# Kernel optimization log

Measured on AMD Instinct MI355X. Metric: run time of the kernel, lower is better.

Reference implementation:

```python
import jax, jax.numpy as jnp
import numpy as np

H, DK, DV, S = 16, 1024, 1024, 2048
DH_QK = DK // H  # 64, per-head q/k dim
DH_V = DV // H   # 64, per-head v dim


def setup_inputs() -> dict:
    key = jax.random.key(0)
    ks = jax.random.split(key, 11)
    init = lambda k, shape, fan_in: jax.random.uniform(k, shape, jnp.float32, -1.0, 1.0) / jnp.sqrt(jnp.float32(fan_in))
    return {
        "Q": jax.random.normal(ks[0], (S, DK), jnp.float32),
        "K": jax.random.normal(ks[1], (S, DK), jnp.float32),
        "V": jax.random.normal(ks[2], (S, DV), jnp.float32),
        # per-head Linear weights, torch convention [out, in] stacked over heads
        "Wq": init(ks[3], (H, DH_QK, DH_QK), DH_QK),
        "bq": init(ks[4], (H, DH_QK), DH_QK),
        "Wk": init(ks[5], (H, DH_QK, DH_QK), DH_QK),
        "bk": init(ks[6], (H, DH_QK), DH_QK),
        "Wv": init(ks[7], (H, DH_V, DH_V), DH_V),
        "bv": init(ks[8], (H, DH_V), DH_V),
        "Wo": init(ks[9], (DK, H * DH_V), H * DH_V),  # final linear: d_model x (h*dv_h)
        "bo": init(ks[10], (DK,), H * DH_V),
    }


def reference(Q, K, V, Wq, bq, Wk, bk, Wv, bv, Wo, bo):
    h, dh = Wq.shape[0], Wq.shape[2]
    dv = Wv.shape[2]
    s = Q.shape[0]
    # split features into h per-head chunks (same as slicing loop in torch)
    Qh = Q.reshape(s, h, dh)
    Kh = K.reshape(s, h, dh)
    Vh = V.reshape(s, h, dv)
    # per-head Linear: x @ W.T + b, batched over heads
    q = jnp.einsum('shd,hed->she', Qh, Wq) + bq
    k = jnp.einsum('shd,hed->she', Kh, Wk) + bk
    v = jnp.einsum('shd,hed->she', Vh, Wv) + bv
    # scaled dot-product attention per head
    scores = jnp.einsum('she,the->hst', q, k) / jnp.sqrt(jnp.float32(dh))
    attn = jax.nn.softmax(scores, axis=-1)
    o = jnp.einsum('hst,the->she', attn, v)  # [s, h, dv]
    concat = o.reshape(s, h * dv)
    return concat @ Wo.T + bo
```

## Files before the change

kernel.cpp:

```cpp
#include <hip/hip_runtime.h>
#include <stdint.h>

static constexpr int H   = 16;
static constexpr int S   = 2048;
static constexpr int DHd = 64;
static constexpr int DM  = 1024;
static constexpr int NSPLIT = 4;
static constexpr int KT_PER_SPLIT = (S / 64) / NSPLIT;

using f32x4   = __attribute__((ext_vector_type(4))) float;
using f32x8   = __attribute__((ext_vector_type(8))) float;
using f32x16  = __attribute__((ext_vector_type(16))) float;
using short8  = __attribute__((ext_vector_type(8))) short;
using bf16x8  = __attribute__((ext_vector_type(8))) __bf16;
using uint4v  = __attribute__((ext_vector_type(4))) unsigned int;

#if __has_builtin(__builtin_amdgcn_exp2f)
#define EXP2F __builtin_amdgcn_exp2f
#else
#define EXP2F exp2f
#endif

__device__ __forceinline__ short f2bf(float f) {
  union { float f; uint32_t u; } v; v.f = f;
  uint32_t r = v.u + 0x7FFFu + ((v.u >> 16) & 1u);
  return (short)(r >> 16);
}
__device__ __forceinline__ float bf2f(short s) {
  union { uint32_t u; float f; } v;
  v.u = ((uint32_t)(unsigned short)s) << 16;
  return v.f;
}

__device__ __forceinline__ short8 f2bf8(f32x4 a, f32x4 b) {
  short8 v;
  v[0] = f2bf(a[0]); v[1] = f2bf(a[1]); v[2] = f2bf(a[2]); v[3] = f2bf(a[3]);
  v[4] = f2bf(b[0]); v[5] = f2bf(b[1]); v[6] = f2bf(b[2]); v[7] = f2bf(b[3]);
  return v;
}

__device__ __forceinline__ unsigned int pkbf(float a, float b) {
  __bf16 x = (__bf16)a, y = (__bf16)b;
  unsigned short ux = __builtin_bit_cast(unsigned short, x);
  unsigned short uy = __builtin_bit_cast(unsigned short, y);
  return (unsigned int)ux | ((unsigned int)uy << 16);
}

__device__ __forceinline__ f32x4 mfma16(short8 a, short8 b, f32x4 c) {
  return __builtin_amdgcn_mfma_f32_16x16x32_bf16(
      __builtin_bit_cast(bf16x8, a), __builtin_bit_cast(bf16x8, b), c, 0, 0, 0);
}
__device__ __forceinline__ f32x16 mfma32(short8 a, short8 b, f32x16 c) {
  return __builtin_amdgcn_mfma_f32_32x32x16_bf16(
      __builtin_bit_cast(bf16x8, a), __builtin_bit_cast(bf16x8, b), c, 0, 0, 0);
}

__device__ __forceinline__ short8 lds_read_swz(const short* base, int row, int chunk) {
  return *(const short8*)((const char*)base + row * 128 + ((chunk ^ (row & 7)) << 4));
}
__device__ __forceinline__ void lds_write_swz(short* base, int row, int chunk, short8 v) {
  *(short8*)((char*)base + row * 128 + ((chunk ^ (row & 7)) << 4)) = v;
}

using u32g = __attribute__((address_space(1))) const unsigned int;
using u32l = __attribute__((address_space(3))) unsigned int;
__device__ __forceinline__ void gl_lds16(const short* g, short* l) {
  __builtin_amdgcn_global_load_lds(
      reinterpret_cast<u32g*>(reinterpret_cast<uintptr_t>(g)),
      reinterpret_cast<u32l*>(static_cast<unsigned int>(reinterpret_cast<uintptr_t>(l))),
      16, 0, 0);
}

__global__ __launch_bounds__(256) void proj_kernel(
    const float* __restrict__ Q, const float* __restrict__ K, const float* __restrict__ V,
    const float* __restrict__ Wq, const float* __restrict__ bq,
    const float* __restrict__ Wk, const float* __restrict__ bk,
    const float* __restrict__ Wv, const float* __restrict__ bv,
    const float* __restrict__ Wo, short* __restrict__ wob,
    short* __restrict__ qb, short* __restrict__ kb, short* __restrict__ vtb) {
  const int t = threadIdx.x;
  const int mode = blockIdx.z;

  if (mode == 3) {
    int chunk = blockIdx.y * gridDim.x + blockIdx.x;
    int i = (chunk * 256 + t) * 16;
    f32x4 x0 = *(const f32x4*)(Wo + i);
    f32x4 x1 = *(const f32x4*)(Wo + i + 4);
    f32x4 x2 = *(const f32x4*)(Wo + i + 8);
    f32x4 x3 = *(const f32x4*)(Wo + i + 12);
    *(short8*)(wob + i)     = f2bf8(x0, x1);
    *(short8*)(wob + i + 8) = f2bf8(x2, x3);
    return;
  }

  const int h  = blockIdx.y;
  const int rt = blockIdx.x * 128;

  const float* X; const float* W; const float* bias;
  if (mode == 0)      { X = Q; W = Wq; bias = bq; }
  else if (mode == 1) { X = K; W = Wk; bias = bk; }
  else                { X = V; W = Wv; bias = bv; }
  bias += h * DHd;
  const float scale = (mode == 0) ? 0.125f * 1.44269504f : 1.0f;

  __shared__ short Xs[128 * 64];
  __shared__ short Ws[64 * 64];
  __shared__ short Ot[128 * 72];

#pragma unroll
  for (int p = 0; p < 4; p++) {
    int ci = p * 256 + t;
    int row = ci >> 3, oct = ci & 7;
    const float* g = X + (size_t)(rt + row) * DM + h * DHd + oct * 8;
    f32x4 x0 = *(const f32x4*)g;
    f32x4 x1 = *(const f32x4*)(g + 4);
    lds_write_swz(Xs, row, oct, f2bf8(x0, x1));
  }
#pragma unroll
  for (int p = 0; p < 2; p++) {
    int ci = p * 256 + t;
    int row = ci >> 3, oct = ci & 7;
    const float* g = W + (size_t)h * DHd * DHd + row * DHd + oct * 8;
    f32x4 x0 = *(const f32x4*)g;
    f32x4 x1 = *(const f32x4*)(g + 4);
    lds_write_swz(Ws, row, oct, f2bf8(x0, x1));
  }
  __syncthreads();

  const int wid = t >> 6, lane = t & 63;
  const int l15 = lane & 15, l4 = lane >> 4;

  f32x4 acc[2][4] = {};
#pragma unroll
  for (int ks = 0; ks < 2; ks++) {
    int chunk = ks * 4 + l4;
    short8 a0 = lds_read_swz(Xs, wid * 32 + l15, chunk);
    short8 a1 = lds_read_swz(Xs, wid * 32 + 16 + l15, chunk);
#pragma unroll
    for (int nf = 0; nf < 4; nf++) {
      short8 b = lds_read_swz(Ws, nf * 16 + l15, chunk);
      acc[0][nf] = mfma16(a0, b, acc[0][nf]);
      acc[1][nf] = mfma16(a1, b, acc[1][nf]);
    }
  }

  if (mode < 2) {
    short* out = (mode == 0) ? qb : kb;
#pragma unroll
    for (int mf = 0; mf < 2; mf++)
#pragma unroll
      for (int nf = 0; nf < 4; nf++) {
        int col = nf * 16 + l15;
        float b = bias[col];
#pragma unroll
        for (int r = 0; r < 4; r++) {
          int lrow = wid * 32 + mf * 16 + l4 * 4 + r;
          Ot[lrow * 72 + col] = f2bf((acc[mf][nf][r] + b) * scale);
        }
      }
    __syncthreads();
#pragma unroll
    for (int p = 0; p < 4; p++) {
      int ci = p * 256 + t;
      int row = ci >> 3, c8 = ci & 7;
      short8 v = *(const short8*)&Ot[row * 72 + c8 * 8];
      *(short8*)(out + ((size_t)h * S + rt + row) * DHd + c8 * 8) = v;
    }
  } else {
#pragma unroll
    for (int mf = 0; mf < 2; mf++)
#pragma unroll
      for (int nf = 0; nf < 4; nf++) {
        int col = nf * 16 + l15;
        float b = bias[col];
#pragma unroll
        for (int r = 0; r < 4; r++) {
          int lrow = wid * 32 + mf * 16 + l4 * 4 + r;
          Ot[col * 136 + lrow] = f2bf(acc[mf][nf][r] + b);
        }
      }
    __syncthreads();
#pragma unroll
    for (int p = 0; p < 2; p++) {
      int ci = p * 256 + t;
      int e = ci >> 3, c16 = ci & 7;
      short8 a = *(const short8*)&Ot[e * 136 + c16 * 16];
      short8 b = *(const short8*)&Ot[e * 136 + c16 * 16 + 8];
      short8 lo, hi;
      lo[0] = a[0]; lo[1] = a[1]; lo[2] = a[2]; lo[3] = a[3];
      lo[4] = b[0]; lo[5] = b[1]; lo[6] = b[2]; lo[7] = b[3];
      hi[0] = a[4]; hi[1] = a[5]; hi[2] = a[6]; hi[3] = a[7];
      hi[4] = b[4]; hi[5] = b[5]; hi[6] = b[6]; hi[7] = b[7];
      short* dst = vtb + ((size_t)h * DHd + e) * S + rt + c16 * 16;
      *(short8*)dst       = lo;
      *(short8*)(dst + 8) = hi;
    }
  }
}

__global__ __launch_bounds__(256, 2) void attn_kernel(
    const short* __restrict__ qb, const short* __restrict__ kb,
    const short* __restrict__ vtb, short* __restrict__ OpT,
    float* __restrict__ lbuf) {
  const int h  = blockIdx.x;
  const int sp = blockIdx.y;
  const int t = threadIdx.x, wid = t >> 6, lane = t & 63;
  const int l31 = lane & 31, l5 = lane >> 5;
  const int qw = blockIdx.z * 256 + wid * 64;

  __shared__ short Ks[3][64 * 64];
  __shared__ short Vs[3][64 * 64];

  short8 qf[2][4];
#pragma unroll
  for (int tt = 0; tt < 2; tt++) {
    const short* qrow = qb + ((size_t)h * S + qw + tt * 32 + l31) * DHd;
#pragma unroll
    for (int c = 0; c < 4; c++) qf[tt][c] = *(const short8*)(qrow + c * 16 + l5 * 8);
  }

  const int srow8 = lane >> 3, schunk = lane & 7;
  const int r0 = wid * 16 + srow8, r1 = r0 + 8;
  const int kt0 = sp * KT_PER_SPLIT;
  const short* kg0 = kb + ((size_t)h * S + (size_t)kt0 * 64 + r0) * DHd + ((schunk ^ (r0 & 7)) * 8);
  const short* kg1 = kb + ((size_t)h * S + (size_t)kt0 * 64 + r1) * DHd + ((schunk ^ (r1 & 7)) * 8);
  const short* vg0 = vtb + ((size_t)h * DHd + r0) * S + (size_t)kt0 * 64 + ((schunk ^ (r0 & 7)) * 8);
  const short* vg1 = vtb + ((size_t)h * DHd + r1) * S + (size_t)kt0 * 64 + ((schunk ^ (r1 & 7)) * 8);

  auto stage = [&](int buf, int kk) {
    const size_t ka = (size_t)kk * 64 * DHd;
    const size_t va = (size_t)kk * 64;
    gl_lds16(kg0 + ka, &Ks[buf][wid * 1024]);
    gl_lds16(kg1 + ka, &Ks[buf][wid * 1024 + 512]);
    gl_lds16(vg0 + va, &Vs[buf][wid * 1024]);
    gl_lds16(vg1 + va, &Vs[buf][wid * 1024 + 512]);
  };

  stage(0, 0);
  stage(1, 1);

  f32x16 oa00 = {}, oa01 = {}, oa10 = {}, oa11 = {};
  f32x8 lac0 = {}, lac1 = {};

  for (int kk = 0; kk < KT_PER_SPLIT; kk++) {
    const int cur = kk % 3;
    if (kk + 1 < KT_PER_SPLIT) asm volatile("s_waitcnt vmcnt(4)" ::: "memory");
    else                       asm volatile("s_waitcnt vmcnt(0)" ::: "memory");
    __syncthreads();
    if (kk + 2 < KT_PER_SPLIT) stage((kk + 2) % 3, kk + 2);

    f32x16 s00 = {}, s01 = {}, s10 = {}, s11 = {};
    __builtin_amdgcn_s_setprio(1);
#pragma unroll
    for (int c = 0; c < 4; c++) {
      short8 ak0 = lds_read_swz(Ks[cur], l31, 2 * c + l5);
      short8 ak1 = lds_read_swz(Ks[cur], 32 + l31, 2 * c + l5);
      s00 = mfma32(ak0, qf[0][c], s00);
      s01 = mfma32(ak1, qf[0][c], s01);
      s10 = mfma32(ak0, qf[1][c], s10);
      s11 = mfma32(ak1, qf[1][c], s11);
    }
    __builtin_amdgcn_s_setprio(0);

#pragma unroll
    for (int i = 0; i < 16; i++) {
      float p00 = EXP2F(s00[i]), p01 = EXP2F(s01[i]);
      float p10 = EXP2F(s10[i]), p11 = EXP2F(s11[i]);
      s00[i] = p00; s01[i] = p01; s10[i] = p10; s11[i] = p11;
      lac0[i & 7] += p00 + p01;
      lac1[i & 7] += p10 + p11;
    }

    unsigned int pk0[2][8], pk1[2][8];
#pragma unroll
    for (int g = 0; g < 4; g++) {
      pk0[0][g * 2 + 0] = pkbf(s00[4 * g + 0], s00[4 * g + 1]);
      pk0[0][g * 2 + 1] = pkbf(s00[4 * g + 2], s00[4 * g + 3]);
      pk0[1][g * 2 + 0] = pkbf(s01[4 * g + 0], s01[4 * g + 1]);
      pk0[1][g * 2 + 1] = pkbf(s01[4 * g + 2], s01[4 * g + 3]);
      pk1[0][g * 2 + 0] = pkbf(s10[4 * g + 0], s10[4 * g + 1]);
      pk1[0][g * 2 + 1] = pkbf(s10[4 * g + 2], s10[4 * g + 3]);
      pk1[1][g * 2 + 0] = pkbf(s11[4 * g + 0], s11[4 * g + 1]);
      pk1[1][g * 2 + 1] = pkbf(s11[4 * g + 2], s11[4 * g + 3]);
    }

    __builtin_amdgcn_s_setprio(1);
#pragma unroll
    for (int j = 0; j < 4; j++) {
      const int bb = j >> 1;
      const int s4 = (j & 1) * 4;
      short8 av0 = lds_read_swz(Vs[cur], l31, 2 * j + l5);
      short8 av1 = lds_read_swz(Vs[cur], 32 + l31, 2 * j + l5);
      uint4v pf0, pf1;
      pf0[0] = pk0[bb][s4 + 0]; pf0[1] = pk0[bb][s4 + 1];
      pf0[2] = pk0[bb][s4 + 2]; pf0[3] = pk0[bb][s4 + 3];
      pf1[0] = pk1[bb][s4 + 0]; pf1[1] = pk1[bb][s4 + 1];
      pf1[2] = pk1[bb][s4 + 2]; pf1[3] = pk1[bb][s4 + 3];
      short8 p0 = __builtin_bit_cast(short8, pf0);
      short8 p1 = __builtin_bit_cast(short8, pf1);
      oa00 = mfma32(av0, p0, oa00);
      oa01 = mfma32(av1, p0, oa01);
      oa10 = mfma32(av0, p1, oa10);
      oa11 = mfma32(av1, p1, oa11);
    }
    __builtin_amdgcn_s_setprio(0);
  }

#pragma unroll
  for (int st = 4; st >= 1; st >>= 1)
#pragma unroll
    for (int i = 0; i < st; i++) { lac0[i] += lac0[i + st]; lac1[i] += lac1[i + st]; }
  float l0 = lac0[0] + __shfl_xor(lac0[0], 32);
  float l1 = lac1[0] + __shfl_xor(lac1[0], 32);

#pragma unroll
  for (int r = 0; r < 16; r++) {
    int dvb = (r & 3) + 8 * (r >> 2) + 4 * l5;
    size_t base = (((size_t)sp * H + h) * DHd + dvb) * S + qw + l31;
    OpT[base]            = f2bf(oa00[r]);
    OpT[base + 32UL * S] = f2bf(oa01[r]);
    OpT[base + 32]            = f2bf(oa10[r]);
    OpT[base + 32UL * S + 32] = f2bf(oa11[r]);
  }
  if (l5 == 0) {
    lbuf[((size_t)sp * H + h) * S + qw + l31]      = l0;
    lbuf[((size_t)sp * H + h) * S + qw + 32 + l31] = l1;
  }
}

__global__ __launch_bounds__(256) void combine_kernel(
    const short* __restrict__ OpT, const float* __restrict__ lbuf,
    short* __restrict__ Ob) {
  const int h  = blockIdx.y;
  const int s0 = blockIdx.x * 64;
  __shared__ short tile[64][72];

  const int t = threadIdx.x;
  const int dvh = t >> 3;
  const int sb  = (t & 7) * 8;

  float lt[8] = {};
#pragma unroll
  for (int sp = 0; sp < NSPLIT; sp++) {
    const float* lp = lbuf + ((size_t)sp * H + h) * S + s0 + sb;
    f32x4 a = *(const f32x4*)lp;
    f32x4 b = *(const f32x4*)(lp + 4);
#pragma unroll
    for (int i = 0; i < 4; i++) { lt[i] += a[i]; lt[4 + i] += b[i]; }
  }
  float inv[8];
#pragma unroll
  for (int i = 0; i < 8; i++) inv[i] = 1.0f / lt[i];

#pragma unroll
  for (int half = 0; half < 2; half++) {
    const int dv = dvh + half * 32;
    float acc[8] = {};
#pragma unroll
    for (int sp = 0; sp < NSPLIT; sp++) {
      const short* op = OpT + (((size_t)sp * H + h) * DHd + dv) * S + s0 + sb;
      short8 v = *(const short8*)op;
#pragma unroll
      for (int i = 0; i < 8; i++) acc[i] += bf2f(v[i]);
    }
#pragma unroll
    for (int i = 0; i < 8; i++)
      tile[sb + i][dv] = f2bf(acc[i] * inv[i]);
  }
  __syncthreads();

#pragma unroll
  for (int i = 0; i < 2; i++) {
    int cid = t + i * 256;
    int r = cid >> 3, c = cid & 7;
    short8 v = *(const short8*)&tile[r][c * 8];
    *(short8*)(Ob + (size_t)(s0 + r) * DM + h * DHd + c * 8) = v;
  }
}

__global__ __launch_bounds__(256) void out_gemm(
    const short* __restrict__ Ob, const short* __restrict__ wob,
    const float* __restrict__ bo, float* __restrict__ out) {
  const int m0 = blockIdx.x * 64;
  const int n0 = blockIdx.y * 64;
  constexpr int KT = DM / 64;

  __shared__ short As[3][64 * 64];
  __shared__ short Bs[3][64 * 64];

  const int t = threadIdx.x, wid = t >> 6, lane = t & 63;
  const int l31 = lane & 31, l5 = lane >> 5;
  const int wr = wid >> 1, wn = wid & 1;
  const int srow8 = lane >> 3, schunk = lane & 7;
  const int r0 = wid * 16 + srow8, r1 = r0 + 8;

  const short* ag0 = Ob  + (size_t)(m0 + r0) * DM + ((schunk ^ (r0 & 7)) * 8);
  const short* ag1 = Ob  + (size_t)(m0 + r1) * DM + ((schunk ^ (r1 & 7)) * 8);
  const short* bg0 = wob + (size_t)(n0 + r0) * DM + ((schunk ^ (r0 & 7)) * 8);
  const short* bg1 = wob + (size_t)(n0 + r1) * DM + ((schunk ^ (r1 & 7)) * 8);

  auto stage = [&](int buf, int kc) {
    const int off = kc * 64;
    gl_lds16(ag0 + off, &As[buf][wid * 1024]);
    gl_lds16(ag1 + off, &As[buf][wid * 1024 + 512]);
    gl_lds16(bg0 + off, &Bs[buf][wid * 1024]);
    gl_lds16(bg1 + off, &Bs[buf][wid * 1024 + 512]);
  };

  stage(0, 0);
  stage(1, 1);

  f32x16 acc = {};
  for (int kc = 0; kc < KT; kc++) {
    const int cur = kc % 3;
    if (kc + 1 < KT) asm volatile("s_waitcnt vmcnt(4)" ::: "memory");
    else             asm volatile("s_waitcnt vmcnt(0)" ::: "memory");
    __syncthreads();
    if (kc + 2 < KT) stage((kc + 2) % 3, kc + 2);
#pragma unroll
    for (int c = 0; c < 4; c++) {
      short8 a = lds_read_swz(As[cur], wr * 32 + l31, 2 * c + l5);
      short8 b = lds_read_swz(Bs[cur], wn * 32 + l31, 2 * c + l5);
      acc = mfma32(a, b, acc);
    }
  }
  const int col = n0 + wn * 32 + l31;
  const float bb = bo[col];
#pragma unroll
  for (int r = 0; r < 16; r++) {
    int row = m0 + wr * 32 + (r & 3) + 8 * (r >> 2) + 4 * l5;
    out[(size_t)row * DM + col] = acc[r] + bb;
  }
}

extern "C" void kernel_launch(void* const* d_in, const int* in_sizes, int n_in,
                              void* d_out, int out_size, void* d_ws, size_t ws_size,
                              hipStream_t stream) {
  const float* Q  = (const float*)d_in[0];
  const float* K  = (const float*)d_in[1];
  const float* V  = (const float*)d_in[2];
  const float* Wq = (const float*)d_in[3];
  const float* bq = (const float*)d_in[4];
  const float* Wk = (const float*)d_in[5];
  const float* bk = (const float*)d_in[6];
  const float* Wv = (const float*)d_in[7];
  const float* bv = (const float*)d_in[8];
  const float* Wo = (const float*)d_in[9];
  const float* bo = (const float*)d_in[10];

  char* ws = (char*)d_ws;
  short* qb   = (short*)(ws);
  short* kb   = (short*)(ws + ((size_t)4 << 20));
  short* vtb  = (short*)(ws + ((size_t)8 << 20));
  short* Obf  = (short*)(ws + ((size_t)12 << 20));
  short* wob  = (short*)(ws + ((size_t)16 << 20));
  short* OpT  = (short*)(ws + ((size_t)18 << 20));
  float* lbuf = (float*)(ws + ((size_t)34 << 20));

  proj_kernel<<<dim3(S / 128, H, 4), 256, 0, stream>>>(Q, K, V, Wq, bq, Wk, bk, Wv, bv,
                                                       Wo, wob, qb, kb, vtb);
  attn_kernel<<<dim3(H, NSPLIT, S / 256), 256, 0, stream>>>(qb, kb, vtb, OpT, lbuf);
  combine_kernel<<<dim3(S / 64, H), 256, 0, stream>>>(OpT, lbuf, Obf);
  out_gemm<<<dim3(S / 64, DM / 64), 256, 0, stream>>>(Obf, wob, bo, (float*)d_out);
}
```

Before: 52.42 us.

## Fuse split-K combine into attention kernel via last-block atomic counter

Removes the separate combine kernel launch. Each attention block now bumps a per-(head, query-block) atomic counter after writing its partial output and row sums. The last split to finish reduces all splits and writes the bf16 output tile, reusing the K shared-memory buffer as the transpose tile. A memset of the counters is added each call. The combine work is serialized onto a few tail blocks, which trades launch overhead and a kernel boundary for possible tail imbalance and extra fences.

```diff
diff --git a/kernel.cpp b/kernel.cpp
--- a/kernel.cpp
+++ b/kernel.cpp
@@ -7,6 +7,7 @@
 static constexpr int DM  = 1024;
 static constexpr int NSPLIT = 4;
 static constexpr int KT_PER_SPLIT = (S / 64) / NSPLIT;
+static constexpr int NQBLK = S / 256;
 
 using f32x4   = __attribute__((ext_vector_type(4))) float;
 using f32x8   = __attribute__((ext_vector_type(8))) float;
@@ -201,15 +202,18 @@
 __global__ __launch_bounds__(256, 2) void attn_kernel(
     const short* __restrict__ qb, const short* __restrict__ kb,
     const short* __restrict__ vtb, short* __restrict__ OpT,
-    float* __restrict__ lbuf) {
+    float* __restrict__ lbuf, int* __restrict__ cnt,
+    short* __restrict__ Ob) {
   const int h  = blockIdx.x;
   const int sp = blockIdx.y;
+  const int zb = blockIdx.z;
   const int t = threadIdx.x, wid = t >> 6, lane = t & 63;
   const int l31 = lane & 31, l5 = lane >> 5;
-  const int qw = blockIdx.z * 256 + wid * 64;
+  const int qw = zb * 256 + wid * 64;
 
   __shared__ short Ks[3][64 * 64];
   __shared__ short Vs[3][64 * 64];
+  __shared__ int last_flag;
 
   short8 qf[2][4];
 #pragma unroll
@@ -326,55 +330,62 @@
     lbuf[((size_t)sp * H + h) * S + qw + l31]      = l0;
     lbuf[((size_t)sp * H + h) * S + qw + 32 + l31] = l1;
   }
-}
-
-__global__ __launch_bounds__(256) void combine_kernel(
-    const short* __restrict__ OpT, const float* __restrict__ lbuf,
-    short* __restrict__ Ob) {
-  const int h  = blockIdx.y;
-  const int s0 = blockIdx.x * 64;
-  __shared__ short tile[64][72];
-
-  const int t = threadIdx.x;
+
+  __threadfence();
+  if (t == 0) {
+    int prev = atomicAdd(&cnt[h * NQBLK + zb], 1);
+    last_flag = (prev == NSPLIT - 1);
+  }
+  __syncthreads();
+  if (!last_flag) return;
+  __threadfence();
+
+  short* tile = &Ks[0][0];
   const int dvh = t >> 3;
   const int sb  = (t & 7) * 8;
 
-  float lt[8] = {};
-#pragma unroll
-  for (int sp = 0; sp < NSPLIT; sp++) {
-    const float* lp = lbuf + ((size_t)sp * H + h) * S + s0 + sb;
-    f32x4 a = *(const f32x4*)lp;
-    f32x4 b = *(const f32x4*)(lp + 4);
-#pragma unroll
-    for (int i = 0; i < 4; i++) { lt[i] += a[i]; lt[4 + i] += b[i]; }
-  }
-  float inv[8];
-#pragma unroll
-  for (int i = 0; i < 8; i++) inv[i] = 1.0f / lt[i];
-
-#pragma unroll
-  for (int half = 0; half < 2; half++) {
-    const int dv = dvh + half * 32;
-    float acc[8] = {};
-#pragma unroll
-    for (int sp = 0; sp < NSPLIT; sp++) {
-      const short* op = OpT + (((size_t)sp * H + h) * DHd + dv) * S + s0 + sb;
-      short8 v = *(const short8*)op;
-#pragma unroll
-      for (int i = 0; i < 8; i++) acc[i] += bf2f(v[i]);
-    }
-#pragma unroll
-    for (int i = 0; i < 8; i++)
-      tile[sb + i][dv] = f2bf(acc[i] * inv[i]);
-  }
-  __syncthreads();
-
-#pragma unroll
-  for (int i = 0; i < 2; i++) {
-    int cid = t + i * 256;
-    int r = cid >> 3, c = cid & 7;
-    short8 v = *(const short8*)&tile[r][c * 8];
-    *(short8*)(Ob + (size_t)(s0 + r) * DM + h * DHd + c * 8) = v;
+#pragma unroll
+  for (int sub = 0; sub < 4; sub++) {
+    const int s0 = zb * 256 + sub * 64;
+
+    float lt[8] = {};
+#pragma unroll
+    for (int spp = 0; spp < NSPLIT; spp++) {
+      const float* lp = lbuf + ((size_t)spp * H + h) * S + s0 + sb;
+      f32x4 a = *(const f32x4*)lp;
+      f32x4 b = *(const f32x4*)(lp + 4);
+#pragma unroll
+      for (int i = 0; i < 4; i++) { lt[i] += a[i]; lt[4 + i] += b[i]; }
+    }
+    float inv[8];
+#pragma unroll
+    for (int i = 0; i < 8; i++) inv[i] = 1.0f / lt[i];
+
+#pragma unroll
+    for (int half = 0; half < 2; half++) {
+      const int dv = dvh + half * 32;
+      float acc[8] = {};
+#pragma unroll
+      for (int spp = 0; spp < NSPLIT; spp++) {
+        const short* op = OpT + (((size_t)spp * H + h) * DHd + dv) * S + s0 + sb;
+        short8 v = *(const short8*)op;
+#pragma unroll
+        for (int i = 0; i < 8; i++) acc[i] += bf2f(v[i]);
+      }
+#pragma unroll
+      for (int i = 0; i < 8; i++)
+        tile[(sb + i) * 72 + dv] = f2bf(acc[i] * inv[i]);
+    }
+    __syncthreads();
+
+#pragma unroll
+    for (int i = 0; i < 2; i++) {
+      int cid = t + i * 256;
+      int r = cid >> 3, c = cid & 7;
+      short8 v = *(const short8*)&tile[r * 72 + c * 8];
+      *(short8*)(Ob + (size_t)(s0 + r) * DM + h * DHd + c * 8) = v;
+    }
+    __syncthreads();
   }
 }
 
@@ -456,10 +467,13 @@
   short* wob  = (short*)(ws + ((size_t)16 << 20));
   short* OpT  = (short*)(ws + ((size_t)18 << 20));
   float* lbuf = (float*)(ws + ((size_t)34 << 20));
+  int*   cnt  = (int*)(ws + ((size_t)34 << 20) + (512 << 10));
+
+  hipMemsetAsync(cnt, 0, H * NQBLK * sizeof(int), stream);
 
   proj_kernel<<<dim3(S / 128, H, 4), 256, 0, stream>>>(Q, K, V, Wq, bq, Wk, bk, Wv, bv,
                                                        Wo, wob, qb, kb, vtb);
-  attn_kernel<<<dim3(H, NSPLIT, S / 256), 256, 0, stream>>>(qb, kb, vtb, OpT, lbuf);
-  combine_kernel<<<dim3(S / 64, H), 256, 0, stream>>>(OpT, lbuf, Obf);
+  attn_kernel<<<dim3(H, NSPLIT, S / 256), 256, 0, stream>>>(qb, kb, vtb, OpT, lbuf,
+                                                            cnt, Obf);
   out_gemm<<<dim3(S / 64, DM / 64), 256, 0, stream>>>(Obf, wob, bo, (float*)d_out);
 }
```

Result: slower. 133.7 us (+155.0%).
